# Optimization experiments

Hardware: AMD Instinct MI355X
Metric: run time of the kernel (lower is better)

The kernel has to match this reference:

```python
import jax, jax.numpy as jnp
import numpy as np

G0, G1, G2 = 128, 64, 32
N0, N1, N2 = 800_000, 200_000, 32_768
EPS = 1e-5
OFFS = np.array([[i, j, k] for i in (0, 1) for j in (0, 1) for k in (0, 1)], np.int64)  # octant order, idx = 4i+2j+k


def _flat(c, G):
    return (c[..., 0] * G + c[..., 1]) * G + c[..., 2]


def _unflat(k, G):
    return np.stack([k // (G * G), (k // G) % G, k % G], -1)


def _child_map(cc, keys_fine, Gf):
    # for each coarse voxel, indices of its 8 fine children (masked if absent)
    k = _flat(2 * cc[:, None, :] + OFFS[None], Gf)  # [M,8]
    pos = np.clip(np.searchsorted(keys_fine, k), 0, len(keys_fine) - 1)
    valid = keys_fine[pos] == k
    return np.where(valid, pos, 0).astype(np.int32), valid


def _parent_map(cf, keys_coarse, Gc):
    pos = np.searchsorted(keys_coarse, _flat(cf // 2, Gc)).astype(np.int32)
    off = ((cf % 2) @ np.array([4, 2, 1])).astype(np.int32)
    return pos, off


def _build():
    rng = np.random.default_rng(0)
    keys2 = np.arange(G2 ** 3, dtype=np.int64)          # coarsest level fully active
    c2 = _unflat(keys2, G2)
    forced1 = _flat(2 * c2 + rng.integers(0, 2, (len(c2), 3)), G1)  # >=1 child per parent
    occ = np.zeros(G1 ** 3, bool); occ[forced1] = True
    extra1 = rng.choice(np.flatnonzero(~occ), N1 - len(forced1), replace=False)
    keys1 = np.sort(np.concatenate([forced1, extra1]))
    c1 = _unflat(keys1, G1)
    cand = _flat((2 * c1[:, None, :] + OFFS[None]).reshape(-1, 3), G0)  # children of active level1
    forced0 = _flat(2 * c1 + rng.integers(0, 2, (N1, 3)), G0)
    occf = np.zeros(G0 ** 3, bool); occf[forced0] = True
    occc = np.zeros(G0 ** 3, bool); occc[cand] = True
    extra0 = rng.choice(np.flatnonzero(occc & ~occf), N0 - N1, replace=False)
    keys0 = np.sort(np.concatenate([forced0, extra0]))
    c0 = _unflat(keys0, G0)
    idx_up1, mask_up1 = _child_map(c1, keys0, G0)
    idx_up2, mask_up2 = _child_map(c2, keys1, G1)
    par_d2, off_d2 = _parent_map(c1, keys2, G2)   # output coords = level1 (x_up1)
    par_d1, off_d1 = _parent_map(c0, keys1, G1)   # output coords = level0 (x)
    return idx_up1, mask_up1, idx_up2, mask_up2, par_d2, off_d2, par_d1, off_d1


def setup_inputs() -> dict:
    key = jax.random.key(0)
    ks = jax.random.split(key, 5)
    idx_up1, mask_up1, idx_up2, mask_up2, par_d2, off_d2, par_d1, off_d1 = _build()
    C0, C1, C2 = 32, 64, 128
    return {
        "x": jax.random.normal(ks[0], (N0, C0), jnp.float32),
        "W_up1": jax.random.normal(ks[1], (8, C0, C1), jnp.float32) / np.sqrt(8 * C0),
        "W_up2": jax.random.normal(ks[2], (8, C1, C2), jnp.float32) / np.sqrt(8 * C1),
        "W_d2": jax.random.normal(ks[3], (8, C2, C1), jnp.float32) / np.sqrt(C2),
        "W_d1": jax.random.normal(ks[4], (8, C1, C0), jnp.float32) / np.sqrt(C1),
        "g1": jnp.ones((C1,), jnp.float32), "b1": jnp.zeros((C1,), jnp.float32),
        "g2": jnp.ones((C2,), jnp.float32), "b2": jnp.zeros((C2,), jnp.float32),
        "g3": jnp.ones((C1,), jnp.float32), "b3": jnp.zeros((C1,), jnp.float32),
        "g4": jnp.ones((C0,), jnp.float32), "b4": jnp.zeros((C0,), jnp.float32),
        "idx_up1": jnp.asarray(idx_up1), "mask_up1": jnp.asarray(mask_up1),
        "idx_up2": jnp.asarray(idx_up2), "mask_up2": jnp.asarray(mask_up2),
        "par_d2": jnp.asarray(par_d2), "off_d2": jnp.asarray(off_d2),
        "par_d1": jnp.asarray(par_d1), "off_d1": jnp.asarray(off_d1),
    }


def _sconv(f, idx, mask, W):
    # stride-2 k=2 sparse conv: gather 8 children then per-offset GEMM
    g = f[idx] * mask[..., None].astype(f.dtype)        # [M,8,Cin]
    return jnp.einsum('mki,kio->mo', g, W)


def _tconv(f, par, off, W):
    # transposed stride-2 k=2: each fine voxel gets one parent, octant selects weight
    fp = f[par]                                          # [M,Cin]
    out = jnp.zeros((fp.shape[0], W.shape[2]), f.dtype)
    for k in range(8):                                   # fixed 8-way kernel loop
        out = out + jnp.where((off == k)[:, None], fp @ W[k], 0.0)
    return out


def _inorm(f, g, b):
    # instance norm over active voxels (single instance), per channel, biased var
    mu = f.mean(0)
    var = f.var(0)
    return (f - mu) * jax.lax.rsqrt(var + EPS) * g + b


def reference(x, W_up1, W_up2, W_d2, W_d1, g1, b1, g2, b2, g3, b3, g4, b4,
              idx_up1, mask_up1, idx_up2, mask_up2, par_d2, off_d2, par_d1, off_d1):
    x_up1 = _inorm(_sconv(x, idx_up1, mask_up1, W_up1), g1, b1)
    x_up2 = _inorm(_sconv(x_up1, idx_up2, mask_up2, W_up2), g2, b2)
    x_down1 = _inorm(_tconv(x_up2, par_d2, off_d2, W_d2), g3, b3)
    x_down2 = _inorm(_tconv(x_down1, par_d1, off_d1, W_d1), g4, b4)
    return (x_down2, x_down1, x_up2, x_up1)
```

## Files before the change

### kernel.cpp

```cpp
#include <hip/hip_runtime.h>
#include <cstdint>
#include <cstddef>

#define EPS_V 1e-5f
#define SLOTS 16

typedef __attribute__((ext_vector_type(8))) short bf16x8;
typedef __attribute__((ext_vector_type(4))) float f32x4;

__device__ __forceinline__ unsigned short f2b(float f) {
    unsigned u = __float_as_uint(f);
    u = (u + 0x7FFFu + ((u >> 16) & 1u)) >> 16;
    return (unsigned short)u;
}

__device__ __forceinline__ bf16x8 cvt8(float4 a, float4 b) {
    bf16x8 r;
    r[0] = (short)f2b(a.x); r[1] = (short)f2b(a.y);
    r[2] = (short)f2b(a.z); r[3] = (short)f2b(a.w);
    r[4] = (short)f2b(b.x); r[5] = (short)f2b(b.y);
    r[6] = (short)f2b(b.z); r[7] = (short)f2b(b.w);
    return r;
}

__device__ __forceinline__ float b2f(unsigned short u) {
    return __uint_as_float((unsigned)u << 16);
}

__device__ __forceinline__ void b2f8(bf16x8 v, float4& a, float4& b) {
    a.x = b2f((unsigned short)v[0]); a.y = b2f((unsigned short)v[1]);
    a.z = b2f((unsigned short)v[2]); a.w = b2f((unsigned short)v[3]);
    b.x = b2f((unsigned short)v[4]); b.y = b2f((unsigned short)v[5]);
    b.z = b2f((unsigned short)v[6]); b.w = b2f((unsigned short)v[7]);
}

__device__ __forceinline__ float4 nrm4(float4 v, const float* ss, const float* tt, int c) {
    v.x = fmaf(v.x, ss[c + 0], tt[c + 0]);
    v.y = fmaf(v.y, ss[c + 1], tt[c + 1]);
    v.z = fmaf(v.z, ss[c + 2], tt[c + 2]);
    v.w = fmaf(v.w, ss[c + 3], tt[c + 3]);
    return v;
}

__device__ __forceinline__ void ntst(float* p, float4 v) {
    f32x4 w; w[0] = v.x; w[1] = v.y; w[2] = v.z; w[3] = v.w;
    __builtin_nontemporal_store(w, (f32x4*)p);
}

__device__ __forceinline__ void slot_sum(const float* st, int c, float& s0, float& s1) {
    s0 = 0.f; s1 = 0.f;
    #pragma unroll
    for (int s = 0; s < SLOTS; s++) {
        s0 += st[s * 256 + c];
        s1 += st[s * 256 + 128 + c];
    }
}

template <int C>
__device__ __forceinline__ void mk_norm(const float* st_in, int Min,
                                        const float* gw, const float* bw,
                                        float* ss, float* tt) {
    if (threadIdx.x < C) {
        int c = threadIdx.x;
        float s0, s1; slot_sum(st_in, c, s0, s1);
        float invM = 1.0f / (float)Min;
        float mu = s0 * invM;
        float var = fmaf(s1, invM, -mu * mu);
        float s = rsqrtf(var + EPS_V) * gw[c];
        ss[c] = s; tt[c] = fmaf(-mu, s, bw[c]);
    }
}

__global__ void k_detect(const unsigned int* __restrict__ w, int nwords,
                         int* __restrict__ flag) {
    unsigned loc = 0;
    for (int i = threadIdx.x; i < nwords; i += blockDim.x)
        if (w[i] > 1u) loc = 1u;
    if (loc) atomicOr(flag, 1);
}

__device__ __forceinline__ void pack_one(const void* mask, int r, int isByte,
                                         unsigned char* pm) {
    unsigned byte = 0;
    if (isByte) {
        const unsigned char* mb = (const unsigned char*)mask;
        #pragma unroll
        for (int k = 0; k < 8; k++) byte |= (mb[(size_t)r * 8 + k] ? 1u : 0u) << k;
    } else {
        const int* mi = (const int*)mask;
        #pragma unroll
        for (int k = 0; k < 8; k++) byte |= (mi[(size_t)r * 8 + k] ? 1u : 0u) << k;
    }
    pm[r] = (unsigned char)byte;
}

__device__ __forceinline__ void wshuf_one(const float* W, int Cin, int Cout,
                                          unsigned short* dst, int g) {
    int KB = Cin >> 5, NB = Cout >> 4;
    int L = g & 63;
    int rest = g >> 6;
    int nb = rest % NB; rest /= NB;
    int kb = rest % KB; int t = rest / KB;
    int q = L >> 4, col = nb * 16 + (L & 15);
    const float* src = W + ((size_t)t * Cin + kb * 32 + q * 8) * Cout + col;
    unsigned short* d = dst + (size_t)g * 8;
    #pragma unroll
    for (int j = 0; j < 8; j++) d[j] = f2b(src[(size_t)j * Cout]);
}

__global__ __launch_bounds__(256)
void k_prep(const void* msk1, int M1, const void* msk2, int M2,
            const int* __restrict__ flag,
            unsigned char* __restrict__ pm1, unsigned char* __restrict__ pm2,
            const float* __restrict__ W1, const float* __restrict__ W2,
            const float* __restrict__ W3, const float* __restrict__ W4,
            unsigned short* __restrict__ ws1, unsigned short* __restrict__ ws2,
            unsigned short* __restrict__ ws3, unsigned short* __restrict__ ws4,
            const int* __restrict__ par2, int* __restrict__ wmax2,
            const int* __restrict__ par1, int* __restrict__ wmax1,
            int N0, int do_wmax) {
    int P1 = (M1 + 255) >> 8, P2 = (M2 + 255) >> 8;
    int b = blockIdx.x, tid = threadIdx.x;
    if (b < P1) { int r = b * 256 + tid; if (r < M1) pack_one(msk1, r, *flag, pm1); return; }
    b -= P1;
    if (b < P2) { int r = b * 256 + tid; if (r < M2) pack_one(msk2, r, *flag, pm2); return; }
    b -= P2;
    if (b < 8)  { wshuf_one(W1, 32, 64,  ws1, b * 256 + tid); return; }
    b -= 8;
    if (b < 32) { wshuf_one(W2, 64, 128, ws2, b * 256 + tid); return; }
    b -= 32;
    if (b < 32) { wshuf_one(W3, 128, 64, ws3, b * 256 + tid); return; }
    b -= 32;
    if (b < 8)  { wshuf_one(W4, 64, 32,  ws4, b * 256 + tid); return; }
    b -= 8;
    if (!do_wmax) return;
    if (b < P1) { int r = b * 256 + tid; if (r < M1) atomicMax(&wmax2[par2[r]], r + 1); return; }
    b -= P1;
    { int r = b * 256 + tid; if (r < N0) atomicMax(&wmax1[par1[r]], r + 1); }
}


__global__ __launch_bounds__(256)
void k_conv1b(const float* __restrict__ xin, const unsigned short* __restrict__ Wsh,
              const int* __restrict__ idx, const unsigned char* __restrict__ pm,
              unsigned short* __restrict__ rawout, float* __restrict__ st, int M) {
    __shared__ float ls[2 * 64];
    if (threadIdx.x < 128) ls[threadIdx.x] = 0.f;
    __syncthreads();
    const int lane = threadIdx.x & 63, wid = threadIdx.x >> 6;
    const int q = lane >> 4, li = lane & 15;
    int tile = blockIdx.x * 4 + wid;
    float sum[4] = {0, 0, 0, 0}, sq[4] = {0, 0, 0, 0};
    if (tile * 16 < M) {
        int rowA = tile * 16 + li;
        unsigned m = pm[rowA];
        const int4* ipv = (const int4*)(idx + (size_t)rowA * 8);
        int4 ia = ipv[0], ib = ipv[1];
        int ipr[8] = {ia.x, ia.y, ia.z, ia.w, ib.x, ib.y, ib.z, ib.w};
        float4 F0[8], F1[8];
        #pragma unroll
        for (int t = 0; t < 8; t++) {
            const float4* p = (const float4*)(xin + (size_t)ipr[t] * 32 + q * 8);
            F0[t] = p[0]; F1[t] = p[1];
        }
        f32x4 acc[4];
        #pragma unroll
        for (int nb = 0; nb < 4; nb++) acc[nb] = (f32x4)0.f;
        bf16x8 z8 = (bf16x8)(short)0;
        #pragma unroll
        for (int t = 0; t < 8; t++) {
            bool valid = (m >> t) & 1u;
            bf16x8 av = valid ? cvt8(F0[t], F1[t]) : z8;
            #pragma unroll
            for (int nb = 0; nb < 4; nb++) {
                bf16x8 bb = *(const bf16x8*)(Wsh + ((size_t)(t * 4 + nb) * 64 + lane) * 8);
                acc[nb] = __builtin_amdgcn_mfma_f32_16x16x32_bf16(av, bb, acc[nb], 0, 0, 0);
            }
        }
        int rowD = tile * 16 + q * 4;
        #pragma unroll
        for (int nb = 0; nb < 4; nb++)
            #pragma unroll
            for (int r = 0; r < 4; r++) {
                float v = acc[nb][r];
                rawout[(size_t)(rowD + r) * 64 + nb * 16 + li] = f2b(v);
                sum[nb] += v; sq[nb] = fmaf(v, v, sq[nb]);
            }
    }
    #pragma unroll
    for (int nb = 0; nb < 4; nb++) {
        int c = nb * 16 + li;
        atomicAdd(&ls[c], sum[nb]); atomicAdd(&ls[64 + c], sq[nb]);
    }
    __syncthreads();
    int slot = (blockIdx.x & (SLOTS - 1)) << 8;
    if (threadIdx.x < 64) {
        atomicAdd(&st[slot + threadIdx.x], ls[threadIdx.x]);
        atomicAdd(&st[slot + 128 + threadIdx.x], ls[64 + threadIdx.x]);
    }
}

__global__ __launch_bounds__(256)
void k_conv2b(const unsigned short* __restrict__ rin, const unsigned short* __restrict__ Wsh,
              const int* __restrict__ idx, const unsigned char* __restrict__ pm,
              unsigned short* __restrict__ rawout, float* __restrict__ st, int M,
              const float* __restrict__ st_in, const float* __restrict__ gw,
              const float* __restrict__ bw, int Min, float* __restrict__ nout) {
    __shared__ float ls[2 * 128];
    __shared__ float ss[64], tt[64];
    ls[threadIdx.x] = 0.f;
    mk_norm<64>(st_in, Min, gw, bw, ss, tt);
    __syncthreads();
    const int lane = threadIdx.x & 63, wid = threadIdx.x >> 6;
    const int q = lane >> 4, li = lane & 15;
    int tile = blockIdx.x * 4 + wid;
    int rowA = tile * 16 + li;
    unsigned m = pm[rowA];
    const int4* ipv = (const int4*)(idx + (size_t)rowA * 8);
    int4 ia = ipv[0], ib = ipv[1];
    int ipr[8] = {ia.x, ia.y, ia.z, ia.w, ib.x, ib.y, ib.z, ib.w};
    bf16x8 Ga[8], Gb[8];
    #pragma unroll
    for (int t = 0; t < 8; t++) {
        const unsigned short* base = rin + (size_t)ipr[t] * 64;
        Ga[t] = *(const bf16x8*)(base + q * 8);
        Gb[t] = *(const bf16x8*)(base + 32 + q * 8);
    }
    f32x4 acc[8];
    #pragma unroll
    for (int nb = 0; nb < 8; nb++) acc[nb] = (f32x4)0.f;
    bf16x8 z8 = (bf16x8)(short)0;
    #pragma unroll
    for (int t = 0; t < 8; t++) {
        bool valid = (m >> t) & 1u;
        float4 f0, f1, f2, f3;
        b2f8(Ga[t], f0, f1); b2f8(Gb[t], f2, f3);
        int c0 = q * 8;
        f0 = nrm4(f0, ss, tt, c0);      f1 = nrm4(f1, ss, tt, c0 + 4);
        f2 = nrm4(f2, ss, tt, 32 + c0); f3 = nrm4(f3, ss, tt, 32 + c0 + 4);
        if (valid) {
            float* dpp = nout + (size_t)ipr[t] * 64;
            ntst(dpp + q * 8, f0);      ntst(dpp + q * 8 + 4, f1);
            ntst(dpp + 32 + q * 8, f2); ntst(dpp + 32 + q * 8 + 4, f3);
        }
        bf16x8 a0 = valid ? cvt8(f0, f1) : z8;
        bf16x8 a1 = valid ? cvt8(f2, f3) : z8;
        #pragma unroll
        for (int nb = 0; nb < 8; nb++) {
            bf16x8 b0 = *(const bf16x8*)(Wsh + ((size_t)(t * 16 + nb) * 64 + lane) * 8);
            acc[nb] = __builtin_amdgcn_mfma_f32_16x16x32_bf16(a0, b0, acc[nb], 0, 0, 0);
            bf16x8 b1 = *(const bf16x8*)(Wsh + ((size_t)(t * 16 + 8 + nb) * 64 + lane) * 8);
            acc[nb] = __builtin_amdgcn_mfma_f32_16x16x32_bf16(a1, b1, acc[nb], 0, 0, 0);
        }
    }
    int rowD = tile * 16 + q * 4;
    float sum[8], sq[8];
    #pragma unroll
    for (int nb = 0; nb < 8; nb++) {
        sum[nb] = 0.f; sq[nb] = 0.f;
        #pragma unroll
        for (int r = 0; r < 4; r++) {
            float v = acc[nb][r];
            rawout[(size_t)(rowD + r) * 128 + nb * 16 + li] = f2b(v);
            sum[nb] += v; sq[nb] = fmaf(v, v, sq[nb]);
        }
    }
    #pragma unroll
    for (int nb = 0; nb < 8; nb++) {
        int c = nb * 16 + li;
        atomicAdd(&ls[c], sum[nb]); atomicAdd(&ls[128 + c], sq[nb]);
    }
    __syncthreads();
    int slot = (blockIdx.x & (SLOTS - 1)) << 8;
    if (threadIdx.x < 128) {
        atomicAdd(&st[slot + threadIdx.x], ls[threadIdx.x]);
        atomicAdd(&st[slot + 128 + threadIdx.x], ls[128 + threadIdx.x]);
    }
}

__global__ __launch_bounds__(256)
void k_conv3b(const unsigned short* __restrict__ rin, const unsigned short* __restrict__ Wsh,
              const int* __restrict__ par, const int* __restrict__ off,
              unsigned short* __restrict__ rawout, float* __restrict__ st, int M,
              const float* __restrict__ st_in, const float* __restrict__ gw,
              const float* __restrict__ bw, int Min, float* __restrict__ nout,
              const int* __restrict__ wmax) {
    __shared__ float ls[2 * 64];
    __shared__ float ss[128], tt[128];
    if (threadIdx.x < 128) ls[threadIdx.x] = 0.f;
    mk_norm<128>(st_in, Min, gw, bw, ss, tt);
    __syncthreads();
    const int lane = threadIdx.x & 63, wid = threadIdx.x >> 6;
    const int q = lane >> 4, li = lane & 15;
    int pid = blockIdx.x * 4 + wid;
    float sum[4] = {0, 0, 0, 0}, sq[4] = {0, 0, 0, 0};
    if (pid * 32 < M) {
        int r0 = pid * 32 + li, r1 = r0 + 16;
        int p0 = par[r0], p1 = par[r1];
        int o0 = off[r0], o1 = off[r1];
        bool w0 = (wmax[p0] == r0 + 1);
        bool w1 = (wmax[p1] == r1 + 1);
        bf16x8 Xa[4], Ya[4];
        #pragma unroll
        for (int kb = 0; kb < 4; kb++) {
            Xa[kb] = *(const bf16x8*)(rin + (size_t)p0 * 128 + kb * 32 + q * 8);
            Ya[kb] = *(const bf16x8*)(rin + (size_t)p1 * 128 + kb * 32 + q * 8);
        }
        bf16x8 A0[4], A1[4];
        #pragma unroll
        for (int kb = 0; kb < 4; kb++) {
            float4 x0, x1, y0, y1;
            b2f8(Xa[kb], x0, x1); b2f8(Ya[kb], y0, y1);
            int c0 = kb * 32 + q * 8;
            x0 = nrm4(x0, ss, tt, c0); x1 = nrm4(x1, ss, tt, c0 + 4);
            y0 = nrm4(y0, ss, tt, c0); y1 = nrm4(y1, ss, tt, c0 + 4);
            if (w0) {
                float* dp = nout + (size_t)p0 * 128 + kb * 32 + q * 8;
                ntst(dp, x0); ntst(dp + 4, x1);
            }
            if (w1) {
                float* dp = nout + (size_t)p1 * 128 + kb * 32 + q * 8;
                ntst(dp, y0); ntst(dp + 4, y1);
            }
            A0[kb] = cvt8(x0, x1);
            A1[kb] = cvt8(y0, y1);
        }
        f32x4 acc0[4], acc1[4];
        #pragma unroll
        for (int nb = 0; nb < 4; nb++) { acc0[nb] = (f32x4)0.f; acc1[nb] = (f32x4)0.f; }
        bf16x8 z8 = (bf16x8)(short)0;
        for (int o = 0; o < 8; o++) {
            bool s0 = (o0 == o), s1 = (o1 == o);
            if (__ballot(s0 || s1) == 0ull) continue;
            bf16x8 M0[4], M1[4];
            #pragma unroll
            for (int kb = 0; kb < 4; kb++) {
                M0[kb] = s0 ? A0[kb] : z8;
                M1[kb] = s1 ? A1[kb] : z8;
            }
            #pragma unroll
            for (int nb = 0; nb < 4; nb++)
                #pragma unroll
                for (int kb = 0; kb < 4; kb++) {
                    bf16x8 bb = *(const bf16x8*)(Wsh + ((((size_t)o * 4 + kb) * 4 + nb) * 64 + lane) * 8);
                    acc0[nb] = __builtin_amdgcn_mfma_f32_16x16x32_bf16(M0[kb], bb, acc0[nb], 0, 0, 0);
                    acc1[nb] = __builtin_amdgcn_mfma_f32_16x16x32_bf16(M1[kb], bb, acc1[nb], 0, 0, 0);
                }
        }
        int d0 = pid * 32 + q * 4, d1 = d0 + 16;
        #pragma unroll
        for (int nb = 0; nb < 4; nb++)
            #pragma unroll
            for (int r = 0; r < 4; r++) {
                float v0 = acc0[nb][r], v1 = acc1[nb][r];
                rawout[(size_t)(d0 + r) * 64 + nb * 16 + li] = f2b(v0);
                rawout[(size_t)(d1 + r) * 64 + nb * 16 + li] = f2b(v1);
                sum[nb] += v0 + v1;
                sq[nb] = fmaf(v0, v0, sq[nb]); sq[nb] = fmaf(v1, v1, sq[nb]);
            }
    }
    #pragma unroll
    for (int nb = 0; nb < 4; nb++) {
        int c = nb * 16 + li;
        atomicAdd(&ls[c], sum[nb]); atomicAdd(&ls[64 + c], sq[nb]);
    }
    __syncthreads();
    int slot = (blockIdx.x & (SLOTS - 1)) << 8;
    if (threadIdx.x < 64) {
        atomicAdd(&st[slot + threadIdx.x], ls[threadIdx.x]);
        atomicAdd(&st[slot + 128 + threadIdx.x], ls[64 + threadIdx.x]);
    }
}

__global__ __launch_bounds__(256)
void k_conv4b(const unsigned short* __restrict__ rin, const unsigned short* __restrict__ Wsh,
              const int* __restrict__ par, const int* __restrict__ off,
              float* __restrict__ out, float* __restrict__ st, int M,
              const float* __restrict__ st_in, const float* __restrict__ gw,
              const float* __restrict__ bw, int Min, float* __restrict__ nout,
              const int* __restrict__ wmax) {
    __shared__ unsigned short Wl[8 * 2 * 2 * 64 * 8];
    __shared__ float ls[2 * 32];
    __shared__ float ss[64], tt[64];
    {
        const int4* s = (const int4*)Wsh; int4* d = (int4*)Wl;
        for (int i = threadIdx.x; i < 2048; i += 256) d[i] = s[i];
    }
    if (threadIdx.x < 64) ls[threadIdx.x & 63] = 0.f;
    mk_norm<64>(st_in, Min, gw, bw, ss, tt);
    __syncthreads();
    const int lane = threadIdx.x & 63, wid = threadIdx.x >> 6;
    const int q = lane >> 4, li = lane & 15;
    int pid = blockIdx.x * 4 + wid;
    float sum[2] = {0, 0}, sq[2] = {0, 0};
    if (pid * 32 < M) {
        int r0 = pid * 32 + li, r1 = r0 + 16;
        int p0 = par[r0], p1 = par[r1];
        int o0 = off[r0], o1 = off[r1];
        bool w0 = (wmax[p0] == r0 + 1);
        bool w1 = (wmax[p1] == r1 + 1);
        bf16x8 Xa[2], Ya[2];
        #pragma unroll
        for (int kb = 0; kb < 2; kb++) {
            Xa[kb] = *(const bf16x8*)(rin + (size_t)p0 * 64 + kb * 32 + q * 8);
            Ya[kb] = *(const bf16x8*)(rin + (size_t)p1 * 64 + kb * 32 + q * 8);
        }
        bf16x8 A0[2], A1[2];
        #pragma unroll
        for (int kb = 0; kb < 2; kb++) {
            float4 x0, x1, y0, y1;
            b2f8(Xa[kb], x0, x1); b2f8(Ya[kb], y0, y1);
            int c0 = kb * 32 + q * 8;
            x0 = nrm4(x0, ss, tt, c0); x1 = nrm4(x1, ss, tt, c0 + 4);
            y0 = nrm4(y0, ss, tt, c0); y1 = nrm4(y1, ss, tt, c0 + 4);
            if (w0) {
                float* dp = nout + (size_t)p0 * 64 + kb * 32 + q * 8;
                ntst(dp, x0); ntst(dp + 4, x1);
            }
            if (w1) {
                float* dp = nout + (size_t)p1 * 64 + kb * 32 + q * 8;
                ntst(dp, y0); ntst(dp + 4, y1);
            }
            A0[kb] = cvt8(x0, x1);
            A1[kb] = cvt8(y0, y1);
        }
        f32x4 acc0[2], acc1[2];
        #pragma unroll
        for (int nb = 0; nb < 2; nb++) { acc0[nb] = (f32x4)0.f; acc1[nb] = (f32x4)0.f; }
        bf16x8 z8 = (bf16x8)(short)0;
        for (int o = 0; o < 8; o++) {
            bool s0 = (o0 == o), s1 = (o1 == o);
            if (__ballot(s0 || s1) == 0ull) continue;
            bf16x8 M0[2], M1[2];
            #pragma unroll
            for (int kb = 0; kb < 2; kb++) {
                M0[kb] = s0 ? A0[kb] : z8;
                M1[kb] = s1 ? A1[kb] : z8;
            }
            #pragma unroll
            for (int nb = 0; nb < 2; nb++)
                #pragma unroll
                for (int kb = 0; kb < 2; kb++) {
                    bf16x8 bb = *(const bf16x8*)&Wl[(((o * 2 + kb) * 2 + nb) * 64 + lane) * 8];
                    acc0[nb] = __builtin_amdgcn_mfma_f32_16x16x32_bf16(M0[kb], bb, acc0[nb], 0, 0, 0);
                    acc1[nb] = __builtin_amdgcn_mfma_f32_16x16x32_bf16(M1[kb], bb, acc1[nb], 0, 0, 0);
                }
        }
        int d0 = pid * 32 + q * 4, d1 = d0 + 16;
        #pragma unroll
        for (int nb = 0; nb < 2; nb++)
            #pragma unroll
            for (int r = 0; r < 4; r++) {
                float v0 = acc0[nb][r], v1 = acc1[nb][r];
                out[(size_t)(d0 + r) * 32 + nb * 16 + li] = v0;
                out[(size_t)(d1 + r) * 32 + nb * 16 + li] = v1;
                sum[nb] += v0 + v1;
                sq[nb] = fmaf(v0, v0, sq[nb]); sq[nb] = fmaf(v1, v1, sq[nb]);
            }
    }
    #pragma unroll
    for (int nb = 0; nb < 2; nb++) {
        int c = nb * 16 + li;
        atomicAdd(&ls[c], sum[nb]); atomicAdd(&ls[32 + c], sq[nb]);
    }
    __syncthreads();
    int slot = (blockIdx.x & (SLOTS - 1)) << 8;
    if (threadIdx.x < 32) {
        atomicAdd(&st[slot + threadIdx.x], ls[threadIdx.x]);
        atomicAdd(&st[slot + 128 + threadIdx.x], ls[32 + threadIdx.x]);
    }
}

__global__ __launch_bounds__(256)
void k_conv1(const float* __restrict__ xin, const unsigned short* __restrict__ Wsh,
             const int* __restrict__ idx, const unsigned char* __restrict__ pm,
             float* __restrict__ out, float* __restrict__ st, int M) {
    __shared__ unsigned short Wl[8 * 4 * 64 * 8];
    __shared__ float ls[2 * 64];
    {
        const int4* s = (const int4*)Wsh; int4* d = (int4*)Wl;
        for (int i = threadIdx.x; i < 2048; i += 256) d[i] = s[i];
    }
    if (threadIdx.x < 128) ls[threadIdx.x] = 0.f;
    __syncthreads();
    const int lane = threadIdx.x & 63, wid = threadIdx.x >> 6;
    const int q = lane >> 4, li = lane & 15;
    int tile = blockIdx.x * 4 + wid;
    float sum[4] = {0, 0, 0, 0}, sq[4] = {0, 0, 0, 0};
    if (tile * 16 < M) {
        int rowA = tile * 16 + li;
        unsigned m = pm[rowA];
        const int4* ipv = (const int4*)(idx + (size_t)rowA * 8);
        int4 ia = ipv[0], ib = ipv[1];
        int ipr[8] = {ia.x, ia.y, ia.z, ia.w, ib.x, ib.y, ib.z, ib.w};
        float4 F0[8], F1[8];
        #pragma unroll
        for (int t = 0; t < 8; t++) {
            const float4* p = (const float4*)(xin + (size_t)ipr[t] * 32 + q * 8);
            F0[t] = p[0]; F1[t] = p[1];
        }
        f32x4 acc[4];
        #pragma unroll
        for (int nb = 0; nb < 4; nb++) acc[nb] = (f32x4)0.f;
        bf16x8 z8 = (bf16x8)(short)0;
        #pragma unroll
        for (int t = 0; t < 8; t++) {
            bool valid = (m >> t) & 1u;
            bf16x8 av = valid ? cvt8(F0[t], F1[t]) : z8;
            #pragma unroll
            for (int nb = 0; nb < 4; nb++) {
                bf16x8 bb = *(const bf16x8*)&Wl[((t * 4 + nb) * 64 + lane) * 8];
                acc[nb] = __builtin_amdgcn_mfma_f32_16x16x32_bf16(av, bb, acc[nb], 0, 0, 0);
            }
        }
        int rowD = tile * 16 + q * 4;
        #pragma unroll
        for (int nb = 0; nb < 4; nb++)
            #pragma unroll
            for (int r = 0; r < 4; r++) {
                float v = acc[nb][r];
                out[(size_t)(rowD + r) * 64 + nb * 16 + li] = v;
                sum[nb] += v; sq[nb] = fmaf(v, v, sq[nb]);
            }
    }
    #pragma unroll
    for (int nb = 0; nb < 4; nb++) {
        int c = nb * 16 + li;
        atomicAdd(&ls[c], sum[nb]); atomicAdd(&ls[64 + c], sq[nb]);
    }
    __syncthreads();
    int slot = (blockIdx.x & (SLOTS - 1)) << 8;
    if (threadIdx.x < 64) {
        atomicAdd(&st[slot + threadIdx.x], ls[threadIdx.x]);
        atomicAdd(&st[slot + 128 + threadIdx.x], ls[64 + threadIdx.x]);
    }
}

__global__ __launch_bounds__(256)
void k_conv2(const float* __restrict__ xin, const unsigned short* __restrict__ Wsh,
             const int* __restrict__ idx, const unsigned char* __restrict__ pm,
             float* __restrict__ out, float* __restrict__ st, int M) {
    __shared__ float ls[2 * 128];
    ls[threadIdx.x] = 0.f;
    __syncthreads();
    const int lane = threadIdx.x & 63, wid = threadIdx.x >> 6;
    const int q = lane >> 4, li = lane & 15;
    int tile = blockIdx.x * 4 + wid;
    int rowA = tile * 16 + li;
    unsigned m = pm[rowA];
    const int4* ipv = (const int4*)(idx + (size_t)rowA * 8);
    int4 ia = ipv[0], ib = ipv[1];
    int ipr[8] = {ia.x, ia.y, ia.z, ia.w, ib.x, ib.y, ib.z, ib.w};
    f32x4 acc[8];
    #pragma unroll
    for (int nb = 0; nb < 8; nb++) acc[nb] = (f32x4)0.f;
    bf16x8 z8 = (bf16x8)(short)0;
    #pragma unroll
    for (int h = 0; h < 2; h++) {
        float4 G[4][4];
        #pragma unroll
        for (int t = 0; t < 4; t++) {
            const float* base = xin + (size_t)ipr[h * 4 + t] * 64;
            const float4* p0 = (const float4*)(base + q * 8);
            const float4* p1 = (const float4*)(base + 32 + q * 8);
            G[t][0] = p0[0]; G[t][1] = p0[1]; G[t][2] = p1[0]; G[t][3] = p1[1];
        }
        #pragma unroll
        for (int t = 0; t < 4; t++) {
            int tp = h * 4 + t;
            bool valid = (m >> tp) & 1u;
            bf16x8 a0 = valid ? cvt8(G[t][0], G[t][1]) : z8;
            bf16x8 a1 = valid ? cvt8(G[t][2], G[t][3]) : z8;
            #pragma unroll
            for (int nb = 0; nb < 8; nb++) {
                bf16x8 b0 = *(const bf16x8*)(Wsh + ((size_t)(tp * 16 + nb) * 64 + lane) * 8);
                acc[nb] = __builtin_amdgcn_mfma_f32_16x16x32_bf16(a0, b0, acc[nb], 0, 0, 0);
                bf16x8 b1 = *(const bf16x8*)(Wsh + ((size_t)(tp * 16 + 8 + nb) * 64 + lane) * 8);
                acc[nb] = __builtin_amdgcn_mfma_f32_16x16x32_bf16(a1, b1, acc[nb], 0, 0, 0);
            }
        }
    }
    int rowD = tile * 16 + q * 4;
    float sum[8], sq[8];
    #pragma unroll
    for (int nb = 0; nb < 8; nb++) {
        sum[nb] = 0.f; sq[nb] = 0.f;
        #pragma unroll
        for (int r = 0; r < 4; r++) {
            float v = acc[nb][r];
            out[(size_t)(rowD + r) * 128 + nb * 16 + li] = v;
            sum[nb] += v; sq[nb] = fmaf(v, v, sq[nb]);
        }
    }
    #pragma unroll
    for (int nb = 0; nb < 8; nb++) {
        int c = nb * 16 + li;
        atomicAdd(&ls[c], sum[nb]); atomicAdd(&ls[128 + c], sq[nb]);
    }
    __syncthreads();
    int slot = (blockIdx.x & (SLOTS - 1)) << 8;
    if (threadIdx.x < 128) {
        atomicAdd(&st[slot + threadIdx.x], ls[threadIdx.x]);
        atomicAdd(&st[slot + 128 + threadIdx.x], ls[128 + threadIdx.x]);
    }
}

__global__ __launch_bounds__(256)
void k_conv3(const float* __restrict__ xin, const unsigned short* __restrict__ Wsh,
             const int* __restrict__ par, const int* __restrict__ off,
             float* __restrict__ out, float* __restrict__ st, int M) {
    __shared__ float ls[2 * 64];
    if (threadIdx.x < 128) ls[threadIdx.x] = 0.f;
    __syncthreads();
    const int lane = threadIdx.x & 63, wid = threadIdx.x >> 6;
    const int q = lane >> 4, li = lane & 15;
    int pid = blockIdx.x * 4 + wid;
    float sum[4] = {0, 0, 0, 0}, sq[4] = {0, 0, 0, 0};
    if (pid * 32 < M) {
        int r0 = pid * 32 + li, r1 = r0 + 16;
        int p0 = par[r0], p1 = par[r1];
        int o0 = off[r0], o1 = off[r1];
        bf16x8 A0[4], A1[4];
        #pragma unroll
        for (int kb = 0; kb < 4; kb++) {
            const float4* pa = (const float4*)(xin + (size_t)p0 * 128 + kb * 32 + q * 8);
            A0[kb] = cvt8(pa[0], pa[1]);
            const float4* pb = (const float4*)(xin + (size_t)p1 * 128 + kb * 32 + q * 8);
            A1[kb] = cvt8(pb[0], pb[1]);
        }
        f32x4 acc0[4], acc1[4];
        #pragma unroll
        for (int nb = 0; nb < 4; nb++) { acc0[nb] = (f32x4)0.f; acc1[nb] = (f32x4)0.f; }
        bf16x8 z8 = (bf16x8)(short)0;
        for (int o = 0; o < 8; o++) {
            bool s0 = (o0 == o), s1 = (o1 == o);
            if (__ballot(s0 || s1) == 0ull) continue;
            bf16x8 M0[4], M1[4];
            #pragma unroll
            for (int kb = 0; kb < 4; kb++) {
                M0[kb] = s0 ? A0[kb] : z8;
                M1[kb] = s1 ? A1[kb] : z8;
            }
            #pragma unroll
            for (int nb = 0; nb < 4; nb++)
                #pragma unroll
                for (int kb = 0; kb < 4; kb++) {
                    bf16x8 bb = *(const bf16x8*)(Wsh + ((((size_t)o * 4 + kb) * 4 + nb) * 64 + lane) * 8);
                    acc0[nb] = __builtin_amdgcn_mfma_f32_16x16x32_bf16(M0[kb], bb, acc0[nb], 0, 0, 0);
                    acc1[nb] = __builtin_amdgcn_mfma_f32_16x16x32_bf16(M1[kb], bb, acc1[nb], 0, 0, 0);
                }
        }
        int d0 = pid * 32 + q * 4, d1 = d0 + 16;
        #pragma unroll
        for (int nb = 0; nb < 4; nb++)
            #pragma unroll
            for (int r = 0; r < 4; r++) {
                float v0 = acc0[nb][r], v1 = acc1[nb][r];
                out[(size_t)(d0 + r) * 64 + nb * 16 + li] = v0;
                out[(size_t)(d1 + r) * 64 + nb * 16 + li] = v1;
                sum[nb] += v0 + v1;
                sq[nb] = fmaf(v0, v0, sq[nb]); sq[nb] = fmaf(v1, v1, sq[nb]);
            }
    }
    #pragma unroll
    for (int nb = 0; nb < 4; nb++) {
        int c = nb * 16 + li;
        atomicAdd(&ls[c], sum[nb]); atomicAdd(&ls[64 + c], sq[nb]);
    }
    __syncthreads();
    int slot = (blockIdx.x & (SLOTS - 1)) << 8;
    if (threadIdx.x < 64) {
        atomicAdd(&st[slot + threadIdx.x], ls[threadIdx.x]);
        atomicAdd(&st[slot + 128 + threadIdx.x], ls[64 + threadIdx.x]);
    }
}

__global__ __launch_bounds__(256)
void k_conv4(const float* __restrict__ xin, const unsigned short* __restrict__ Wsh,
             const int* __restrict__ par, const int* __restrict__ off,
             float* __restrict__ out, float* __restrict__ st, int M) {
    __shared__ unsigned short Wl[8 * 2 * 2 * 64 * 8];
    __shared__ float ls[2 * 32];
    {
        const int4* s = (const int4*)Wsh; int4* d = (int4*)Wl;
        for (int i = threadIdx.x; i < 2048; i += 256) d[i] = s[i];
    }
    if (threadIdx.x < 64) ls[threadIdx.x] = 0.f;
    __syncthreads();
    const int lane = threadIdx.x & 63, wid = threadIdx.x >> 6;
    const int q = lane >> 4, li = lane & 15;
    int pid = blockIdx.x * 4 + wid;
    float sum[2] = {0, 0}, sq[2] = {0, 0};
    if (pid * 32 < M) {
        int r0 = pid * 32 + li, r1 = r0 + 16;
        int p0 = par[r0], p1 = par[r1];
        int o0 = off[r0], o1 = off[r1];
        bf16x8 A0[2], A1[2];
        #pragma unroll
        for (int kb = 0; kb < 2; kb++) {
            const float4* pa = (const float4*)(xin + (size_t)p0 * 64 + kb * 32 + q * 8);
            A0[kb] = cvt8(pa[0], pa[1]);
            const float4* pb = (const float4*)(xin + (size_t)p1 * 64 + kb * 32 + q * 8);
            A1[kb] = cvt8(pb[0], pb[1]);
        }
        f32x4 acc0[2], acc1[2];
        #pragma unroll
        for (int nb = 0; nb < 2; nb++) { acc0[nb] = (f32x4)0.f; acc1[nb] = (f32x4)0.f; }
        bf16x8 z8 = (bf16x8)(short)0;
        for (int o = 0; o < 8; o++) {
            bool s0 = (o0 == o), s1 = (o1 == o);
            if (__ballot(s0 || s1) == 0ull) continue;
            bf16x8 M0[2], M1[2];
            #pragma unroll
            for (int kb = 0; kb < 2; kb++) {
                M0[kb] = s0 ? A0[kb] : z8;
                M1[kb] = s1 ? A1[kb] : z8;
            }
            #pragma unroll
            for (int nb = 0; nb < 2; nb++)
                #pragma unroll
                for (int kb = 0; kb < 2; kb++) {
                    bf16x8 bb = *(const bf16x8*)&Wl[(((o * 2 + kb) * 2 + nb) * 64 + lane) * 8];
                    acc0[nb] = __builtin_amdgcn_mfma_f32_16x16x32_bf16(M0[kb], bb, acc0[nb], 0, 0, 0);
                    acc1[nb] = __builtin_amdgcn_mfma_f32_16x16x32_bf16(M1[kb], bb, acc1[nb], 0, 0, 0);
                }
        }
        int d0 = pid * 32 + q * 4, d1 = d0 + 16;
        #pragma unroll
        for (int nb = 0; nb < 2; nb++)
            #pragma unroll
            for (int r = 0; r < 4; r++) {
                float v0 = acc0[nb][r], v1 = acc1[nb][r];
                out[(size_t)(d0 + r) * 32 + nb * 16 + li] = v0;
                out[(size_t)(d1 + r) * 32 + nb * 16 + li] = v1;
                sum[nb] += v0 + v1;
                sq[nb] = fmaf(v0, v0, sq[nb]); sq[nb] = fmaf(v1, v1, sq[nb]);
            }
    }
    #pragma unroll
    for (int nb = 0; nb < 2; nb++) {
        int c = nb * 16 + li;
        atomicAdd(&ls[c], sum[nb]); atomicAdd(&ls[32 + c], sq[nb]);
    }
    __syncthreads();
    int slot = (blockIdx.x & (SLOTS - 1)) << 8;
    if (threadIdx.x < 32) {
        atomicAdd(&st[slot + threadIdx.x], ls[threadIdx.x]);
        atomicAdd(&st[slot + 128 + threadIdx.x], ls[32 + threadIdx.x]);
    }
}

template <int C>
__global__ __launch_bounds__(256)
void k_norm(float* __restrict__ f, int M, const float* __restrict__ st,
            const float* __restrict__ g, const float* __restrict__ b) {
    __shared__ float sc[C], sh[C];
    if (threadIdx.x < C) {
        int c = threadIdx.x;
        float s0, s1; slot_sum(st, c, s0, s1);
        float invM = 1.0f / (float)M;
        float mu = s0 * invM;
        float var = fmaf(s1, invM, -mu * mu);
        float s = rsqrtf(var + EPS_V) * g[c];
        sc[c] = s;
        sh[c] = fmaf(-mu, s, b[c]);
    }
    __syncthreads();
    const int total = M * (C / 4);
    const int cq = C / 4;
    float4* p = (float4*)f;
    for (int i = blockIdx.x * blockDim.x + threadIdx.x; i < total;
         i += gridDim.x * blockDim.x) {
        float4 v = p[i];
        int c0 = (i % cq) * 4;
        v.x = fmaf(v.x, sc[c0 + 0], sh[c0 + 0]);
        v.y = fmaf(v.y, sc[c0 + 1], sh[c0 + 1]);
        v.z = fmaf(v.z, sc[c0 + 2], sh[c0 + 2]);
        v.w = fmaf(v.w, sc[c0 + 3], sh[c0 + 3]);
        ntst((float*)(p + i), v);
    }
}

extern "C" void kernel_launch(void* const* d_in, const int* in_sizes, int n_in,
                              void* d_out, int out_size, void* d_ws, size_t ws_size,
                              hipStream_t stream) {
    const float* x   = (const float*)d_in[0];
    const float* W1  = (const float*)d_in[1];
    const float* W2  = (const float*)d_in[2];
    const float* W3  = (const float*)d_in[3];
    const float* W4  = (const float*)d_in[4];
    const float* g1  = (const float*)d_in[5];
    const float* b1  = (const float*)d_in[6];
    const float* g2  = (const float*)d_in[7];
    const float* b2  = (const float*)d_in[8];
    const float* g3  = (const float*)d_in[9];
    const float* b3  = (const float*)d_in[10];
    const float* g4  = (const float*)d_in[11];
    const float* b4  = (const float*)d_in[12];
    const int*  idx1 = (const int*)d_in[13];
    const void* msk1 = d_in[14];
    const int*  idx2 = (const int*)d_in[15];
    const void* msk2 = d_in[16];
    const int*  par2 = (const int*)d_in[17];
    const int*  off2 = (const int*)d_in[18];
    const int*  par1 = (const int*)d_in[19];
    const int*  off1 = (const int*)d_in[20];

    const int N1 = in_sizes[17];
    const int N0 = in_sizes[19];
    const int N2 = in_sizes[15] / 8;

    float* outp = (float*)d_out;
    float* sA = outp;
    float* sB = sA + (size_t)N0 * 32;
    float* sC = sB + (size_t)N1 * 64;
    float* sD = sC + (size_t)N2 * 128;

    char* w = (char*)d_ws;
    int*   flag = (int*)w;
    float* st1 = (float*)(w + 256);
    float* st2 = st1 + SLOTS * 256;
    float* st3 = st2 + SLOTS * 256;
    float* st4 = st3 + SLOTS * 256;

    auto al = [](size_t v) { return (v + 255) & ~(size_t)255; };

    size_t o = 256 + (size_t)4 * SLOTS * 256 * 4;
    size_t oWm2 = o; o += (size_t)N2 * 4;
    size_t oWm1 = o; o += (size_t)N1 * 4; o = al(o);
    size_t zEnd = o;
    size_t oS1 = o;  o += 32768;
    size_t oS2 = o;  o += 131072;
    size_t oS3 = o;  o += 131072;
    size_t oS4 = o;  o += 32768;
    size_t oP1 = o;  o += al((size_t)N1);
    size_t oP2 = o;  o += al((size_t)N2); o = al(o);
    size_t oR1 = o;  o += (size_t)N1 * 64 * 2;
    size_t oR2 = o;  o += (size_t)N2 * 128 * 2;
    size_t oR3 = o;  o += (size_t)N1 * 64 * 2;
    size_t need = o;

    const bool fused = (ws_size >= need);

    unsigned short* ws1p = (unsigned short*)(w + oS1);
    unsigned short* ws2p = (unsigned short*)(w + oS2);
    unsigned short* ws3p = (unsigned short*)(w + oS3);
    unsigned short* ws4p = (unsigned short*)(w + oS4);
    unsigned char* pm1 = (unsigned char*)(w + oP1);
    unsigned char* pm2 = (unsigned char*)(w + oP2);
    int* wm2 = (int*)(w + oWm2);
    int* wm1 = (int*)(w + oWm1);
    unsigned short* R1 = (unsigned short*)(w + oR1);
    unsigned short* R2 = (unsigned short*)(w + oR2);
    unsigned short* R3 = (unsigned short*)(w + oR3);

    hipMemsetAsync(d_ws, 0, fused ? zEnd : (256 + (size_t)4 * SLOTS * 256 * 4), stream);

    int nwords = N1 * 8 / 4; if (nwords > 4096) nwords = 4096;
    k_detect<<<1, 256, 0, stream>>>((const unsigned int*)msk1, nwords, flag);

    int P1b = (N1 + 255) / 256, P2b = (N2 + 255) / 256;
    int PW = fused ? (P1b + (N0 + 255) / 256) : 0;
    k_prep<<<P1b + P2b + 80 + PW, 256, 0, stream>>>(
        msk1, N1, msk2, N2, flag, pm1, pm2,
        W1, W2, W3, W4, ws1p, ws2p, ws3p, ws4p,
        par2, wm2, par1, wm1, N0, fused ? 1 : 0);

    if (fused) {
        k_conv1b<<<(N1 / 16 + 3) / 4, 256, 0, stream>>>(x, ws1p, idx1, pm1, R1, st1, N1);
        k_conv2b<<<(N2 / 16) / 4, 256, 0, stream>>>(R1, ws2p, idx2, pm2, R2, st2, N2,
                                                    st1, g1, b1, N1, sD);
        k_conv3b<<<(N1 / 32 + 3) / 4, 256, 0, stream>>>(R2, ws3p, par2, off2, R3, st3, N1,
                                                        st2, g2, b2, N2, sC, wm2);
        k_conv4b<<<(N0 / 32 + 3) / 4, 256, 0, stream>>>(R3, ws4p, par1, off1, sA, st4, N0,
                                                        st3, g3, b3, N1, sB, wm1);
        k_norm<32><<<2048, 256, 0, stream>>>(sA, N0, st4, g4, b4);
    } else {
        k_conv1<<<(N1 / 16 + 3) / 4, 256, 0, stream>>>(x, ws1p, idx1, pm1, sD, st1, N1);
        k_norm<64><<<1024, 256, 0, stream>>>(sD, N1, st1, g1, b1);
        k_conv2<<<(N2 / 16) / 4, 256, 0, stream>>>(sD, ws2p, idx2, pm2, sC, st2, N2);
        k_norm<128><<<512, 256, 0, stream>>>(sC, N2, st2, g2, b2);
        k_conv3<<<(N1 / 32 + 3) / 4, 256, 0, stream>>>(sC, ws3p, par2, off2, sB, st3, N1);
        k_norm<64><<<1024, 256, 0, stream>>>(sB, N1, st3, g3, b3);
        k_conv4<<<(N0 / 32 + 3) / 4, 256, 0, stream>>>(sB, ws4p, par1, off1, sA, st4, N0);
        k_norm<32><<<2048, 256, 0, stream>>>(sA, N0, st4, g4, b4);
    }
}
```

Before: 563.2 us.

## Fold mask detect into prep, swizzle blocks across XCDs, halve tconv rows per wave

The separate mask-format detection kernel is removed and its check is done redundantly inside each mask-packing block of the prep kernel, which drops one launch. Block indices in the four fused conv kernels are remapped so that consecutive tiles land on the same XCD, aiming for better L2 locality. The transposed-conv kernels now process 16 rows per wave instead of 32, with twice as many blocks. Launch bounds now request higher occupancy, trading per-wave ILP and MFMA reuse of weight loads for more resident waves.

```diff
diff --git a/kernel.cpp b/kernel.cpp
--- a/kernel.cpp
+++ b/kernel.cpp
@@ -45,6 +45,13 @@
 __device__ __forceinline__ void ntst(float* p, float4 v) {
     f32x4 w; w[0] = v.x; w[1] = v.y; w[2] = v.z; w[3] = v.w;
     __builtin_nontemporal_store(w, (f32x4*)p);
+}
+
+__device__ __forceinline__ int xswz(int bid, int nB) {
+    int q = nB >> 3, r = nB & 7;
+    int x = bid & 7, i = bid >> 3;
+    int base = (x < r) ? x * (q + 1) : r * (q + 1) + (x - r) * q;
+    return base + i;
 }
 
 __device__ __forceinline__ void slot_sum(const float* st, int c, float& s0, float& s1) {
@@ -71,14 +78,6 @@
     }
 }
 
-__global__ void k_detect(const unsigned int* __restrict__ w, int nwords,
-                         int* __restrict__ flag) {
-    unsigned loc = 0;
-    for (int i = threadIdx.x; i < nwords; i += blockDim.x)
-        if (w[i] > 1u) loc = 1u;
-    if (loc) atomicOr(flag, 1);
-}
-
 __device__ __forceinline__ void pack_one(const void* mask, int r, int isByte,
                                          unsigned char* pm) {
     unsigned byte = 0;
@@ -110,7 +109,6 @@
 
 __global__ __launch_bounds__(256)
 void k_prep(const void* msk1, int M1, const void* msk2, int M2,
-            const int* __restrict__ flag,
             unsigned char* __restrict__ pm1, unsigned char* __restrict__ pm2,
             const float* __restrict__ W1, const float* __restrict__ W2,
             const float* __restrict__ W3, const float* __restrict__ W4,
@@ -119,12 +117,24 @@
             const int* __restrict__ par2, int* __restrict__ wmax2,
             const int* __restrict__ par1, int* __restrict__ wmax1,
             int N0, int do_wmax) {
+    __shared__ int sfl;
     int P1 = (M1 + 255) >> 8, P2 = (M2 + 255) >> 8;
     int b = blockIdx.x, tid = threadIdx.x;
-    if (b < P1) { int r = b * 256 + tid; if (r < M1) pack_one(msk1, r, *flag, pm1); return; }
-    b -= P1;
-    if (b < P2) { int r = b * 256 + tid; if (r < M2) pack_one(msk2, r, *flag, pm2); return; }
-    b -= P2;
+    if (b < P1 + P2) {
+        if (tid == 0) sfl = 0;
+        __syncthreads();
+        const unsigned* wm = (const unsigned*)msk1;
+        int nw = M1 * 2; if (nw > 4096) nw = 4096;
+        unsigned loc = 0;
+        for (int i = tid; i < nw; i += 256) if (wm[i] > 1u) loc = 1u;
+        if (loc) atomicOr(&sfl, 1);
+        __syncthreads();
+        int isB = sfl;
+        if (b < P1) { int r = b * 256 + tid; if (r < M1) pack_one(msk1, r, isB, pm1); }
+        else { int r = (b - P1) * 256 + tid; if (r < M2) pack_one(msk2, r, isB, pm2); }
+        return;
+    }
+    b -= P1 + P2;
     if (b < 8)  { wshuf_one(W1, 32, 64,  ws1, b * 256 + tid); return; }
     b -= 8;
     if (b < 32) { wshuf_one(W2, 64, 128, ws2, b * 256 + tid); return; }
@@ -140,7 +150,7 @@
 }
 
 
-__global__ __launch_bounds__(256)
+__global__ __launch_bounds__(256, 3)
 void k_conv1b(const float* __restrict__ xin, const unsigned short* __restrict__ Wsh,
               const int* __restrict__ idx, const unsigned char* __restrict__ pm,
               unsigned short* __restrict__ rawout, float* __restrict__ st, int M) {
@@ -149,7 +159,8 @@
     __syncthreads();
     const int lane = threadIdx.x & 63, wid = threadIdx.x >> 6;
     const int q = lane >> 4, li = lane & 15;
-    int tile = blockIdx.x * 4 + wid;
+    int gi = xswz(blockIdx.x, gridDim.x);
+    int tile = gi * 4 + wid;
     float sum[4] = {0, 0, 0, 0}, sq[4] = {0, 0, 0, 0};
     if (tile * 16 < M) {
         int rowA = tile * 16 + li;
@@ -200,7 +211,7 @@
     }
 }
 
-__global__ __launch_bounds__(256)
+__global__ __launch_bounds__(256, 3)
 void k_conv2b(const unsigned short* __restrict__ rin, const unsigned short* __restrict__ Wsh,
               const int* __restrict__ idx, const unsigned char* __restrict__ pm,
               unsigned short* __restrict__ rawout, float* __restrict__ st, int M,
@@ -213,7 +224,8 @@
     __syncthreads();
     const int lane = threadIdx.x & 63, wid = threadIdx.x >> 6;
     const int q = lane >> 4, li = lane & 15;
-    int tile = blockIdx.x * 4 + wid;
+    int gi = xswz(blockIdx.x, gridDim.x);
+    int tile = gi * 4 + wid;
     int rowA = tile * 16 + li;
     unsigned m = pm[rowA];
     const int4* ipv = (const int4*)(idx + (size_t)rowA * 8);
@@ -278,7 +290,7 @@
     }
 }
 
-__global__ __launch_bounds__(256)
+__global__ __launch_bounds__(256, 4)
 void k_conv3b(const unsigned short* __restrict__ rin, const unsigned short* __restrict__ Wsh,
               const int* __restrict__ par, const int* __restrict__ off,
               unsigned short* __restrict__ rawout, float* __restrict__ st, int M,
@@ -292,71 +304,58 @@
     __syncthreads();
     const int lane = threadIdx.x & 63, wid = threadIdx.x >> 6;
     const int q = lane >> 4, li = lane & 15;
-    int pid = blockIdx.x * 4 + wid;
+    int gi = xswz(blockIdx.x, gridDim.x);
+    int tile = gi * 4 + wid;
     float sum[4] = {0, 0, 0, 0}, sq[4] = {0, 0, 0, 0};
-    if (pid * 32 < M) {
-        int r0 = pid * 32 + li, r1 = r0 + 16;
-        int p0 = par[r0], p1 = par[r1];
-        int o0 = off[r0], o1 = off[r1];
+    if (tile * 16 < M) {
+        int r0 = tile * 16 + li;
+        int p0 = par[r0];
+        int o0 = off[r0];
         bool w0 = (wmax[p0] == r0 + 1);
-        bool w1 = (wmax[p1] == r1 + 1);
-        bf16x8 Xa[4], Ya[4];
+        bf16x8 Xa[4];
+        #pragma unroll
+        for (int kb = 0; kb < 4; kb++)
+            Xa[kb] = *(const bf16x8*)(rin + (size_t)p0 * 128 + kb * 32 + q * 8);
+        bf16x8 A0[4];
         #pragma unroll
         for (int kb = 0; kb < 4; kb++) {
-            Xa[kb] = *(const bf16x8*)(rin + (size_t)p0 * 128 + kb * 32 + q * 8);
-            Ya[kb] = *(const bf16x8*)(rin + (size_t)p1 * 128 + kb * 32 + q * 8);
-        }
-        bf16x8 A0[4], A1[4];
-        #pragma unroll
-        for (int kb = 0; kb < 4; kb++) {
-            float4 x0, x1, y0, y1;
-            b2f8(Xa[kb], x0, x1); b2f8(Ya[kb], y0, y1);
+            float4 x0, x1;
+            b2f8(Xa[kb], x0, x1);
             int c0 = kb * 32 + q * 8;
             x0 = nrm4(x0, ss, tt, c0); x1 = nrm4(x1, ss, tt, c0 + 4);
-            y0 = nrm4(y0, ss, tt, c0); y1 = nrm4(y1, ss, tt, c0 + 4);
             if (w0) {
                 float* dp = nout + (size_t)p0 * 128 + kb * 32 + q * 8;
                 ntst(dp, x0); ntst(dp + 4, x1);
             }
-            if (w1) {
-                float* dp = nout + (size_t)p1 * 128 + kb * 32 + q * 8;
-                ntst(dp, y0); ntst(dp + 4, y1);
-            }
             A0[kb] = cvt8(x0, x1);
-            A1[kb] = cvt8(y0, y1);
-        }
-        f32x4 acc0[4], acc1[4];
-        #pragma unroll
-        for (int nb = 0; nb < 4; nb++) { acc0[nb] = (f32x4)0.f; acc1[nb] = (f32x4)0.f; }
+        }
+        f32x4 acc0[4];
+        #pragma unroll
+        for (int nb = 0; nb < 4; nb++) acc0[nb] = (f32x4)0.f;
         bf16x8 z8 = (bf16x8)(short)0;
         for (int o = 0; o < 8; o++) {
-            bool s0 = (o0 == o), s1 = (o1 == o);
-            if (__ballot(s0 || s1) == 0ull) continue;
-            bf16x8 M0[4], M1[4];
-            #pragma unroll
-            for (int kb = 0; kb < 4; kb++) {
-                M0[kb] = s0 ? A0[kb] : z8;
-                M1[kb] = s1 ? A1[kb] : z8;
-            }
+            bool s0 = (o0 == o);
+            if (__ballot(s0) == 0ull) continue;
+            bf16x8 M0[4];
+            #pragma unroll
+            for (int kb = 0; kb < 4; kb++) M0[kb] = s0 ? A0[kb] : z8;
             #pragma unroll
             for (int nb = 0; nb < 4; nb++)
                 #pragma unroll
                 for (int kb = 0; kb < 4; kb++) {
                     bf16x8 bb = *(const bf16x8*)(Wsh + ((((size_t)o * 4 + kb) * 4 + nb) * 64 + lane) * 8);
                     acc0[nb] = __builtin_amdgcn_mfma_f32_16x16x32_bf16(M0[kb], bb, acc0[nb], 0, 0, 0);
-                    acc1[nb] = __builtin_amdgcn_mfma_f32_16x16x32_bf16(M1[kb], bb, acc1[nb], 0, 0, 0);
                 }
         }
-        int d0 = pid * 32 + q * 4, d1 = d0 + 16;
+        int d0 = tile * 16 + q * 4;
         #pragma unroll
         for (int nb = 0; nb < 4; nb++)
             #pragma unroll
             for (int r = 0; r < 4; r++) {
-                float v0 = acc0[nb][r], v1 = acc1[nb][r];
+                float v0 = acc0[nb][r];
                 rawout[(size_t)(d0 + r) * 64 + nb * 16 + li] = f2b(v0);
-                rawout[(size_t)(d1 + r) * 64 + nb * 16 + li] = f2b(v1);
-                sum[nb] += v0 + v1;
-                sq[nb] = fmaf(v0, v0, sq[nb]); sq[nb] = fmaf(v1, v1, sq[nb]);
+                sum[nb] += v0;
+                sq[nb] = fmaf(v0, v0, sq[nb]);
             }
     }
     #pragma unroll
@@ -372,7 +371,7 @@
     }
 }
 
-__global__ __launch_bounds__(256)
+__global__ __launch_bounds__(256, 4)
 void k_conv4b(const unsigned short* __restrict__ rin, const unsigned short* __restrict__ Wsh,
               const int* __restrict__ par, const int* __restrict__ off,
               float* __restrict__ out, float* __restrict__ st, int M,
@@ -391,71 +390,58 @@
     __syncthreads();
     const int lane = threadIdx.x & 63, wid = threadIdx.x >> 6;
     const int q = lane >> 4, li = lane & 15;
-    int pid = blockIdx.x * 4 + wid;
+    int gi = xswz(blockIdx.x, gridDim.x);
+    int tile = gi * 4 + wid;
     float sum[2] = {0, 0}, sq[2] = {0, 0};
-    if (pid * 32 < M) {
-        int r0 = pid * 32 + li, r1 = r0 + 16;
-        int p0 = par[r0], p1 = par[r1];
-        int o0 = off[r0], o1 = off[r1];
+    if (tile * 16 < M) {
+        int r0 = tile * 16 + li;
+        int p0 = par[r0];
+        int o0 = off[r0];
         bool w0 = (wmax[p0] == r0 + 1);
-        bool w1 = (wmax[p1] == r1 + 1);
-        bf16x8 Xa[2], Ya[2];
+        bf16x8 Xa[2];
+        #pragma unroll
+        for (int kb = 0; kb < 2; kb++)
+            Xa[kb] = *(const bf16x8*)(rin + (size_t)p0 * 64 + kb * 32 + q * 8);
+        bf16x8 A0[2];
         #pragma unroll
         for (int kb = 0; kb < 2; kb++) {
-            Xa[kb] = *(const bf16x8*)(rin + (size_t)p0 * 64 + kb * 32 + q * 8);
-            Ya[kb] = *(const bf16x8*)(rin + (size_t)p1 * 64 + kb * 32 + q * 8);
-        }
-        bf16x8 A0[2], A1[2];
-        #pragma unroll
-        for (int kb = 0; kb < 2; kb++) {
-            float4 x0, x1, y0, y1;
-            b2f8(Xa[kb], x0, x1); b2f8(Ya[kb], y0, y1);
+            float4 x0, x1;
+            b2f8(Xa[kb], x0, x1);
             int c0 = kb * 32 + q * 8;
             x0 = nrm4(x0, ss, tt, c0); x1 = nrm4(x1, ss, tt, c0 + 4);
-            y0 = nrm4(y0, ss, tt, c0); y1 = nrm4(y1, ss, tt, c0 + 4);
             if (w0) {
                 float* dp = nout + (size_t)p0 * 64 + kb * 32 + q * 8;
                 ntst(dp, x0); ntst(dp + 4, x1);
             }
-            if (w1) {
-                float* dp = nout + (size_t)p1 * 64 + kb * 32 + q * 8;
-                ntst(dp, y0); ntst(dp + 4, y1);
-            }
             A0[kb] = cvt8(x0, x1);
-            A1[kb] = cvt8(y0, y1);
-        }
-        f32x4 acc0[2], acc1[2];
-        #pragma unroll
-        for (int nb = 0; nb < 2; nb++) { acc0[nb] = (f32x4)0.f; acc1[nb] = (f32x4)0.f; }
+        }
+        f32x4 acc0[2];
+        #pragma unroll
+        for (int nb = 0; nb < 2; nb++) acc0[nb] = (f32x4)0.f;
         bf16x8 z8 = (bf16x8)(short)0;
         for (int o = 0; o < 8; o++) {
-            bool s0 = (o0 == o), s1 = (o1 == o);
-            if (__ballot(s0 || s1) == 0ull) continue;
-            bf16x8 M0[2], M1[2];
-            #pragma unroll
-            for (int kb = 0; kb < 2; kb++) {
-                M0[kb] = s0 ? A0[kb] : z8;
-                M1[kb] = s1 ? A1[kb] : z8;
-            }
+            bool s0 = (o0 == o);
+            if (__ballot(s0) == 0ull) continue;
+            bf16x8 M0[2];
+            #pragma unroll
+            for (int kb = 0; kb < 2; kb++) M0[kb] = s0 ? A0[kb] : z8;
             #pragma unroll
             for (int nb = 0; nb < 2; nb++)
                 #pragma unroll
                 for (int kb = 0; kb < 2; kb++) {
                     bf16x8 bb = *(const bf16x8*)&Wl[(((o * 2 + kb) * 2 + nb) * 64 + lane) * 8];
                     acc0[nb] = __builtin_amdgcn_mfma_f32_16x16x32_bf16(M0[kb], bb, acc0[nb], 0, 0, 0);
-                    acc1[nb] = __builtin_amdgcn_mfma_f32_16x16x32_bf16(M1[kb], bb, acc1[nb], 0, 0, 0);
                 }
         }
-        int d0 = pid * 32 + q * 4, d1 = d0 + 16;
+        int d0 = tile * 16 + q * 4;
         #pragma unroll
         for (int nb = 0; nb < 2; nb++)
             #pragma unroll
             for (int r = 0; r < 4; r++) {
-                float v0 = acc0[nb][r], v1 = acc1[nb][r];
+                float v0 = acc0[nb][r];
                 out[(size_t)(d0 + r) * 32 + nb * 16 + li] = v0;
-                out[(size_t)(d1 + r) * 32 + nb * 16 + li] = v1;
-                sum[nb] += v0 + v1;
-                sq[nb] = fmaf(v0, v0, sq[nb]); sq[nb] = fmaf(v1, v1, sq[nb]);
+                sum[nb] += v0;
+                sq[nb] = fmaf(v0, v0, sq[nb]);
             }
     }
     #pragma unroll
@@ -817,7 +803,6 @@
     float* sD = sC + (size_t)N2 * 128;
 
     char* w = (char*)d_ws;
-    int*   flag = (int*)w;
     float* st1 = (float*)(w + 256);
     float* st2 = st1 + SLOTS * 256;
     float* st3 = st2 + SLOTS * 256;
@@ -856,13 +841,10 @@
 
     hipMemsetAsync(d_ws, 0, fused ? zEnd : (256 + (size_t)4 * SLOTS * 256 * 4), stream);
 
-    int nwords = N1 * 8 / 4; if (nwords > 4096) nwords = 4096;
-    k_detect<<<1, 256, 0, stream>>>((const unsigned int*)msk1, nwords, flag);
-
     int P1b = (N1 + 255) / 256, P2b = (N2 + 255) / 256;
     int PW = fused ? (P1b + (N0 + 255) / 256) : 0;
     k_prep<<<P1b + P2b + 80 + PW, 256, 0, stream>>>(
-        msk1, N1, msk2, N2, flag, pm1, pm2,
+        msk1, N1, msk2, N2, pm1, pm2,
         W1, W2, W3, W4, ws1p, ws2p, ws3p, ws4p,
         par2, wm2, par1, wm1, N0, fused ? 1 : 0);
 
@@ -870,9 +852,9 @@
         k_conv1b<<<(N1 / 16 + 3) / 4, 256, 0, stream>>>(x, ws1p, idx1, pm1, R1, st1, N1);
         k_conv2b<<<(N2 / 16) / 4, 256, 0, stream>>>(R1, ws2p, idx2, pm2, R2, st2, N2,
                                                     st1, g1, b1, N1, sD);
-        k_conv3b<<<(N1 / 32 + 3) / 4, 256, 0, stream>>>(R2, ws3p, par2, off2, R3, st3, N1,
+        k_conv3b<<<(N1 / 16 + 3) / 4, 256, 0, stream>>>(R2, ws3p, par2, off2, R3, st3, N1,
                                                         st2, g2, b2, N2, sC, wm2);
-        k_conv4b<<<(N0 / 32 + 3) / 4, 256, 0, stream>>>(R3, ws4p, par1, off1, sA, st4, N0,
+        k_conv4b<<<(N0 / 16 + 3) / 4, 256, 0, stream>>>(R3, ws4p, par1, off1, sA, st4, N0,
                                                         st3, g3, b3, N1, sB, wm1);
         k_norm<32><<<2048, 256, 0, stream>>>(sA, N0, st4, g4, b4);
     } else {
```

Result: slower. 599.4 us (+6.4%).
